# Optimization experiments

Measured on AMD Instinct MI355X. Metric: run time of the kernel, lower is better.

The kernel has to match this reference:

```python
import jax, jax.numpy as jnp
import numpy as np

B, S, D, H, HD = 2, 2048, 1024, 16, 64
K, L = 1024, 4  # num_codes, vq_levels


def setup_inputs() -> dict:
    key = jax.random.key(0)
    ks = jax.random.split(key, 12)
    w = lambda k, shape: jax.random.normal(k, shape, jnp.float32) * 0.02
    return {
        "x": jax.random.normal(ks[0], (B, S, D), jnp.float32),
        "ln1_g": jnp.ones((D,), jnp.float32), "ln1_b": jnp.zeros((D,), jnp.float32),
        "wq": w(ks[1], (D, D)), "wk": w(ks[2], (D, D)), "wv": w(ks[3], (D, D)),
        "wg": w(ks[4], (D, D)), "wo": w(ks[5], (D, D)),
        "ln2_g": jnp.ones((D,), jnp.float32), "ln2_b": jnp.zeros((D,), jnp.float32),
        "w1": w(ks[6], (D, 4 * D)), "b1": jnp.zeros((4 * D,), jnp.float32),
        "w2": w(ks[7], (4 * D, D)), "b2": jnp.zeros((D,), jnp.float32),
        "ln3_g": jnp.ones((D,), jnp.float32), "ln3_b": jnp.zeros((D,), jnp.float32),
        "codebooks": jax.random.uniform(ks[8], (L, K, D), jnp.float32, -1.0 / K, 1.0 / K),
    }


def _ln(x, g, b):
    m = jnp.mean(x, -1, keepdims=True)
    v = jnp.var(x, -1, keepdims=True)
    return (x - m) / jnp.sqrt(v + 1e-5) * g + b


def _rope(x):  # x: [B, S, H, HD]
    hd = x.shape[-1]
    inv = 1.0 / (10000.0 ** (jnp.arange(0, hd, 2, dtype=jnp.float32) / hd))
    t = jnp.arange(x.shape[1], dtype=jnp.float32)
    f = jnp.einsum('i,j->ij', t, inv)               # [S, HD/2]
    emb = jnp.concatenate([f, f], -1)               # [S, HD]
    cos = jnp.cos(emb)[None, :, None, :]
    sin = jnp.sin(emb)[None, :, None, :]
    x1, x2 = jnp.split(x, 2, -1)
    rot = jnp.concatenate([-x2, x1], -1)
    return x * cos + rot * sin


def reference(x, ln1_g, ln1_b, wq, wk, wv, wg, wo, ln2_g, ln2_b,
              w1, b1, w2, b2, ln3_g, ln3_b, codebooks):
    # --- retention sub-block (pre-LN) ---
    h = _ln(x, ln1_g, ln1_b)
    q = (h @ wq).reshape(B, S, H, HD)
    k = (h @ wk).reshape(B, S, H, HD)
    v = (h @ wv).reshape(B, S, H, HD)
    q, k = _rope(q), _rope(k)
    q, k, v = (a.transpose(0, 2, 1, 3) for a in (q, k, v))  # [B,H,S,HD]
    i = jnp.arange(S)
    dmask = jnp.tril(i[:, None] - i[None, :]).astype(jnp.float32)  # [S,S], >=0
    gamma = (1.0 - jnp.exp2(-5.0 - jnp.arange(H, dtype=jnp.float32)))[:, None, None]
    decay = (gamma ** dmask) * jnp.tril(jnp.ones((S, S), jnp.float32))  # [H,S,S]
    ret = jnp.einsum('bhqd,bhkd->bhqk', q, k) / np.sqrt(HD).astype(np.float32) * decay
    o = jnp.einsum('bhqk,bhkd->bhqd', ret, v).transpose(0, 2, 1, 3).reshape(B, S, D)
    g = jax.nn.silu(h @ wg)
    x = x + (o * g) @ wo
    # --- MLP sub-block (pre-LN) ---
    h2 = _ln(x, ln2_g, ln2_b)
    x = x + (jax.nn.gelu(h2 @ w1 + b1, approximate=False) @ w2 + b2)
    # --- residual vector quantizer ---
    xn = _ln(x, ln3_g, ln3_b)
    residual, total = xn, jnp.zeros_like(xn)
    ql, el = 0.0, 0.0
    for lvl in range(L):
        cb = codebooks[lvl]                         # [K, D]
        flat = residual.reshape(-1, D)              # [B*S, D]
        d2 = (jnp.sum(flat ** 2, 1, keepdims=True)
              + jnp.sum(cb ** 2, 1) - 2.0 * flat @ cb.T)
        idx = jnp.argmin(d2, 1)
        quant = cb[idx].reshape(xn.shape)
        ql = ql + jnp.mean((quant - jax.lax.stop_gradient(residual)) ** 2)
        el = el + jnp.mean((jax.lax.stop_gradient(quant) - residual) ** 2)
        total = total + quant
        residual = residual - jax.lax.stop_gradient(quant)
    final = xn + jax.lax.stop_gradient(total - xn)  # straight-through
    return (x + final, ql / L, el / L)
```

## Files before the change

### kernel.cpp

```cpp
#include <hip/hip_runtime.h>
#include <cstdint>
#include <cstddef>

#define DEV __device__ __forceinline__

typedef __attribute__((ext_vector_type(8))) short bf16x8;
typedef __attribute__((ext_vector_type(4))) float f32x4;

typedef const __attribute__((address_space(1))) void gl_void;
typedef __attribute__((address_space(3))) void lds_void;

DEV unsigned short f2bf(float f){
  union { float f; uint32_t u; } v; v.f = f;
  uint32_t r = v.u + 0x7FFFu + ((v.u >> 16) & 1u);
  return (unsigned short)(r >> 16);
}
DEV float bf2f(unsigned short u){
  union { uint32_t u; float f; } v; v.u = ((uint32_t)u) << 16; return v.f;
}
DEV uint32_t packbf2(float a, float b){
  return (uint32_t)f2bf(a) | ((uint32_t)f2bf(b) << 16);
}

__global__ void ln_kernel(const float* __restrict__ x, const float* __restrict__ gw,
                          const float* __restrict__ bw, unsigned short* __restrict__ obf,
                          float* __restrict__ of32)
{
  const int row = blockIdx.x, t = threadIdx.x;
  const float4 v = ((const float4*)(x + (size_t)row*1024))[t];
  float s  = v.x + v.y + v.z + v.w;
  float s2 = v.x*v.x + v.y*v.y + v.z*v.z + v.w*v.w;
  #pragma unroll
  for (int o = 32; o >= 1; o >>= 1){ s += __shfl_down(s, o); s2 += __shfl_down(s2, o); }
  __shared__ float red[8];
  const int w = t >> 6, ln = t & 63;
  if (ln == 0){ red[w] = s; red[4+w] = s2; }
  __syncthreads();
  const float fs  = red[0]+red[1]+red[2]+red[3];
  const float fs2 = red[4]+red[5]+red[6]+red[7];
  const float mean = fs * (1.0f/1024.0f);
  const float var  = fs2 * (1.0f/1024.0f) - mean*mean;
  const float rstd = rsqrtf(var + 1e-5f);
  const float4 gv = ((const float4*)gw)[t];
  const float4 bv = ((const float4*)bw)[t];
  float4 o4;
  o4.x = (v.x-mean)*rstd*gv.x + bv.x;
  o4.y = (v.y-mean)*rstd*gv.y + bv.y;
  o4.z = (v.z-mean)*rstd*gv.z + bv.z;
  o4.w = (v.w-mean)*rstd*gv.w + bv.w;
  if (of32) ((float4*)(of32 + (size_t)row*1024))[t] = o4;
  ushort4 ob; ob.x = f2bf(o4.x); ob.y = f2bf(o4.y); ob.z = f2bf(o4.z); ob.w = f2bf(o4.w);
  ((ushort4*)(obf + (size_t)row*1024))[t] = ob;
}

struct Ptr5 { const float* p[5]; };
__global__ void transpose_cvt5(Ptr5 in, unsigned short* __restrict__ out)
{
  __shared__ float tile[32][33];
  const float* src = in.p[blockIdx.z];
  unsigned short* dst = out + (size_t)blockIdx.z*1048576;
  const int c0 = blockIdx.x*32, r0 = blockIdx.y*32;
  const int tx = threadIdx.x & 31, ty = threadIdx.x >> 5;
  #pragma unroll
  for (int i = 0; i < 32; i += 8)
    tile[ty+i][tx] = src[(size_t)(r0+ty+i)*1024 + c0 + tx];
  __syncthreads();
  #pragma unroll
  for (int i = 0; i < 32; i += 8)
    dst[(size_t)(c0+ty+i)*1024 + r0 + tx] = f2bf(tile[tx][ty+i]);
}

__global__ void transpose_cvt(const float* __restrict__ in, unsigned short* __restrict__ out,
                              int R, int C)
{
  __shared__ float tile[32][33];
  const int c0 = blockIdx.x*32, r0 = blockIdx.y*32;
  const int tx = threadIdx.x & 31, ty = threadIdx.x >> 5;
  #pragma unroll
  for (int i = 0; i < 32; i += 8)
    tile[ty+i][tx] = in[(size_t)(r0+ty+i)*C + c0 + tx];
  __syncthreads();
  #pragma unroll
  for (int i = 0; i < 32; i += 8)
    out[(size_t)(c0+ty+i)*R + r0 + tx] = f2bf(tile[tx][ty+i]);
}

__global__ void cvtnorm_kernel(const float* __restrict__ cb, unsigned short* __restrict__ cbbf,
                               float* __restrict__ cbn2)
{
  const int code = blockIdx.x, t = threadIdx.x;
  const float4 v = ((const float4*)(cb + (size_t)code*1024))[t];
  ushort4 o; o.x = f2bf(v.x); o.y = f2bf(v.y); o.z = f2bf(v.z); o.w = f2bf(v.w);
  ((ushort4*)(cbbf + (size_t)code*1024))[t] = o;
  float s = v.x*v.x + v.y*v.y + v.z*v.z + v.w*v.w;
  #pragma unroll
  for (int off = 32; off >= 1; off >>= 1) s += __shfl_down(s, off);
  __shared__ float red[4];
  if ((t & 63) == 0) red[t >> 6] = s;
  __syncthreads();
  if (t == 0) cbn2[code] = red[0]+red[1]+red[2]+red[3];
}

__global__ void rope_tab(float2* __restrict__ rt)
{
  const int i = blockIdx.x*256 + threadIdx.x;
  const int s = i >> 5, j = i & 31;
  const float ang = (float)s * exp2f(-(float)j * 0.4152410118609203f);
  float sn, cs; sincosf(ang, &sn, &cs);
  rt[i] = make_float2(cs, sn);
}

template<int EPI>
__global__ __launch_bounds__(512, 2) void gemm256(
    const unsigned short* __restrict__ A, const unsigned short* __restrict__ BT,
    unsigned short* __restrict__ C, const float* __restrict__ bias,
    const float2* __restrict__ rt, int M, int N, int K)
{
  __shared__ __align__(16) unsigned short SH[65536];
  const int t = threadIdx.x;
  const int w = t >> 6, ln = t & 63, lg = ln >> 4, lc = ln & 15;
  const int wm = w >> 2, wn = w & 3;
  const int gx = gridDim.x, nwg = gridDim.x * gridDim.y;
  int lin = blockIdx.y * gx + blockIdx.x;
  lin = (lin >> 3) + (lin & 7) * (nwg >> 3);
  const int m0 = (lin / gx) * 256, n0 = (lin % gx) * 256;
  const int NT = K >> 6;
  const int nit = NT >> 1;

  f32x4 acc[2][2][4][2] = {};
  bf16x8 aF[4][2], bF[2][2];

  auto stageHT = [&](int d, int isB, int h, int kt){
    const unsigned short* src = isB ? BT : A;
    const int mb = (isB ? n0 : m0) + h*128;
    const int base16 = isB*4096 + d*2048 + h*1024;
    #pragma unroll
    for (int j = 0; j < 2; ++j){
      const int o = j*512 + t;
      const int wu = o & 63;
      const int r16 = wu >> 2, cu = wu & 3;
      const int s = o >> 6;
      const int rg = s >> 1, cg = s & 1;
      const int row = rg*16 + r16;
      const int srcu = cg*4 + (cu ^ ((r16 & 8) >> 2));
      __builtin_amdgcn_global_load_lds(
        (gl_void*)(src + (size_t)(mb + row)*K + (size_t)kt*64 + srcu*8),
        (lds_void*)&SH[(base16 + j*512 + (t & ~63))*8], 16, 0, 0);
    }
  };

  auto ldA = [&](int d, int mh, int mf, int ks) -> bf16x8 {
    const int u = d*2048 + mh*1024 + ((wm*4+mf)*2 + ks)*64 + lc*4 + (lg ^ ((lc & 8) >> 2));
    return *(const bf16x8*)&SH[u*8];
  };
  auto ldB = [&](int d, int nh, int nf, int ks) -> bf16x8 {
    const int u = 4096 + d*2048 + nh*1024 + ((wn*2+nf)*2 + ks)*64 + lc*4 + (lg ^ ((lc & 8) >> 2));
    return *(const bf16x8*)&SH[u*8];
  };

#define RD_A(d, mh) { _Pragma("unroll") for (int mf = 0; mf < 4; ++mf){ \
    aF[mf][0] = ldA(d, mh, mf, 0); aF[mf][1] = ldA(d, mh, mf, 1); } }
#define RD_B(d, nh) { _Pragma("unroll") for (int nf = 0; nf < 2; ++nf){ \
    bF[nf][0] = ldB(d, nh, nf, 0); bF[nf][1] = ldB(d, nh, nf, 1); } }
#define MM(mh, nh) { \
    __builtin_amdgcn_s_setprio(1); \
    _Pragma("unroll") for (int mf = 0; mf < 4; ++mf) \
      _Pragma("unroll") for (int nf = 0; nf < 2; ++nf){ \
        acc[mh][nh][mf][nf] = __builtin_amdgcn_mfma_f32_16x16x32_bf16(aF[mf][0], bF[nf][0], acc[mh][nh][mf][nf], 0, 0, 0); \
        acc[mh][nh][mf][nf] = __builtin_amdgcn_mfma_f32_16x16x32_bf16(aF[mf][1], bF[nf][1], acc[mh][nh][mf][nf], 0, 0, 0); } \
    __builtin_amdgcn_s_setprio(0); }
#define BAR()   __builtin_amdgcn_s_barrier()
#define LGKM0() asm volatile("s_waitcnt lgkmcnt(0)" ::: "memory")

  stageHT(0,0,0,0); stageHT(0,0,1,0); stageHT(0,1,0,0); stageHT(0,1,1,0);
  stageHT(1,0,0,1); stageHT(1,1,1,1);
  asm volatile("s_waitcnt vmcnt(4)" ::: "memory");
  BAR();

  for (int it = 0; it < nit; ++it){
    const int v = 2*it + 1, up = 2*it + 2, vp = 2*it + 3;
    const bool hu = (up < NT), hv = (vp < NT);

    RD_A(0,0); RD_B(0,0);
    stageHT(1,0,1,v);
    BAR(); LGKM0(); MM(0,0); BAR();

    RD_B(0,1);
    stageHT(1,1,0,v);
    BAR(); LGKM0(); MM(0,1); BAR();

    RD_A(0,1);
    if (hu) stageHT(0,0,0,up);
    BAR(); LGKM0(); MM(1,1); BAR();

    RD_B(0,0);
    if (hu) stageHT(0,1,1,up);
    BAR(); LGKM0(); MM(1,0);
    if (hu) asm volatile("s_waitcnt vmcnt(4)" ::: "memory");
    else    asm volatile("s_waitcnt vmcnt(0)" ::: "memory");
    BAR();

    RD_A(1,0); RD_B(1,0);
    if (hu) stageHT(0,0,1,up);
    BAR(); LGKM0(); MM(0,0); BAR();

    RD_B(1,1);
    if (hu) stageHT(0,1,0,up);
    BAR(); LGKM0(); MM(0,1); BAR();

    RD_A(1,1);
    if (hv) stageHT(1,0,0,vp);
    BAR(); LGKM0(); MM(1,1); BAR();

    RD_B(1,0);
    if (hv) stageHT(1,1,1,vp);
    BAR(); LGKM0(); MM(1,0);
    if (hv) asm volatile("s_waitcnt vmcnt(4)" ::: "memory");
    else    asm volatile("s_waitcnt vmcnt(0)" ::: "memory");
    BAR();
  }
#undef RD_A
#undef RD_B
#undef MM

  const int sect = n0 >> 10;
  unsigned short* outp3 = C + (size_t)sect*4194304;
  const int cb1 = n0 & 1023;
  unsigned short* slab = &SH[wm*4096];

  #pragma unroll
  for (int mh = 0; mh < 2; ++mh){
    #pragma unroll
    for (int mf = 0; mf < 4; ++mf){
      BAR();
      #pragma unroll
      for (int nh = 0; nh < 2; ++nh)
        #pragma unroll
        for (int nf = 0; nf < 2; ++nf)
          #pragma unroll
          for (int r = 0; r < 4; ++r){
            const int rho = lg*4 + r;
            const int c = nh*128 + wn*32 + nf*16 + lc;
            float vv = acc[mh][nh][mf][nf][r];
            if constexpr (EPI == 2){
              vv += bias[n0 + c];
              vv = 0.5f * vv * (1.0f + erff(vv * 0.70710678118654752f));
            }
            if constexpr (EPI == 3){ if (sect == 3) vv = vv * (1.0f / (1.0f + __expf(-vv))); }
            slab[rho*256 + ((((c>>3) ^ (rho&3)))<<3) + (c&7)] = f2bf(vv);
          }
      LGKM0();
      BAR();
      const int rr = ln >> 2;
      const int row = m0 + mh*128 + wm*64 + mf*16 + rr;
      #pragma unroll
      for (int kk = 0; kk < 2; ++kk){
        const int cc = wn*64 + (ln & 3)*16 + kk*8;
        const int u = cc >> 3;
        const bf16x8 vown = *(const bf16x8*)&slab[rr*256 + ((u ^ (rr&3))<<3)];
        if constexpr (EPI == 3){
          if (sect <= 1){
            const bf16x8 vpart = *(const bf16x8*)&slab[rr*256 + (((u^4) ^ (rr&3))<<3)];
            const int s_ = row & 2047;
            union { bf16x8 v; unsigned short s[8]; } ov, pv, res;
            ov.v = vown; pv.v = vpart;
            #pragma unroll
            for (int j = 0; j < 8; ++j){
              const int col = cc + j;
              const float2 cs = rt[(s_ << 5) + (col & 31)];
              const float a = bf2f(ov.s[j]), b = bf2f(pv.s[j]);
              res.s[j] = f2bf((col & 32) ? (a*cs.x + b*cs.y) : (a*cs.x - b*cs.y));
            }
            *(bf16x8*)(outp3 + (size_t)row*1024 + cb1 + cc) = res.v;
          } else {
            *(bf16x8*)(outp3 + (size_t)row*1024 + cb1 + cc) = vown;
          }
        } else {
          *(bf16x8*)(C + (size_t)row*N + n0 + cc) = vown;
        }
      }
    }
  }
#undef BAR
#undef LGKM0
}

template<int EPI, bool BIAS, bool RES, bool OUTBF, int NSPLIT>
__global__ __launch_bounds__(256, 3) void gemm64_bt(
    const unsigned short* __restrict__ A, const unsigned short* __restrict__ BT,
    void* __restrict__ Cv, const float* __restrict__ bias, const float* __restrict__ resid,
    int M, int N, int K)
{
  __shared__ __align__(16) unsigned short As[2][64*64];
  __shared__ __align__(16) unsigned short Bs[2][128*64];
  const int t = threadIdx.x;
  const int w = t >> 6, ln = t & 63, lg = ln >> 4, lc = ln & 15;
  const int gx = gridDim.x, nwg = gridDim.x * gridDim.y;
  int lin = blockIdx.y * gx + blockIdx.x;
  lin = (lin >> 3) + (lin & 7) * (nwg >> 3);
  const int bx = lin % gx, by = lin / gx;
  const int m0 = by * 64, n0 = bx * 128;
  const int wr = (w >> 1) * 32, wc = (w & 1) * 64;
  f32x4 acc[2][4] = {};
  const int nkt = (K >> 6) / NSPLIT;
  const int ktb = (NSPLIT > 1) ? blockIdx.z * nkt : 0;

  auto stage = [&](int buf, int kt){
    #pragma unroll
    for (int c = 0; c < 2; ++c){
      const int chunk = c*256 + t;
      const int row = chunk >> 3;
      const int kb = (((chunk & 7) << 4) ^ ((row & 7) << 4)) >> 1;
      __builtin_amdgcn_global_load_lds(
          (gl_void*)(A + (size_t)(m0+row)*K + (size_t)(ktb+kt)*64 + kb),
          (lds_void*)&As[buf][(c*256 + w*64)*8], 16, 0, 0);
    }
    #pragma unroll
    for (int c = 0; c < 4; ++c){
      const int chunk = c*256 + t;
      const int row = chunk >> 3;
      const int kb = (((chunk & 7) << 4) ^ ((row & 7) << 4)) >> 1;
      __builtin_amdgcn_global_load_lds(
          (gl_void*)(BT + (size_t)(n0+row)*K + (size_t)(ktb+kt)*64 + kb),
          (lds_void*)&Bs[buf][(c*256 + w*64)*8], 16, 0, 0);
    }
  };

  stage(0, 0);
  __syncthreads();
  for (int kt = 0; kt < nkt; ++kt){
    const int cur = kt & 1;
    if (kt + 1 < nkt) stage(cur ^ 1, kt + 1);
    #pragma unroll
    for (int ks = 0; ks < 2; ++ks){
      bf16x8 af[2], bfr[4];
      #pragma unroll
      for (int i = 0; i < 2; ++i){
        const int rowA = wr + i*16 + lc;
        const int colA = (((ks<<6) + (lg<<4)) ^ ((rowA & 7) << 4)) >> 1;
        af[i] = *(const bf16x8*)&As[cur][rowA*64 + colA];
      }
      #pragma unroll
      for (int i = 0; i < 4; ++i){
        const int rowB = wc + i*16 + lc;
        const int colB = (((ks<<6) + (lg<<4)) ^ ((rowB & 7) << 4)) >> 1;
        bfr[i] = *(const bf16x8*)&Bs[cur][rowB*64 + colB];
      }
      #pragma unroll
      for (int m = 0; m < 2; ++m)
        #pragma unroll
        for (int n = 0; n < 4; ++n)
          acc[m][n] = __builtin_amdgcn_mfma_f32_16x16x32_bf16(af[m], bfr[n], acc[m][n], 0, 0, 0);
    }
    __syncthreads();
  }

  if constexpr (EPI == 4){
    #pragma unroll
    for (int m = 0; m < 2; ++m){
      #pragma unroll
      for (int r = 0; r < 4; ++r){
        float best = 3.4e38f; int bi = 0;
        #pragma unroll
        for (int n = 0; n < 4; ++n){
          const int col = n0 + wc + n*16 + lc;
          const float d = bias[col] - 2.0f*acc[m][n][r];
          if (d < best){ best = d; bi = col; }
        }
        #pragma unroll
        for (int o = 1; o < 16; o <<= 1){
          const float ob = __shfl_xor(best, o);
          const int oi = __shfl_xor(bi, o);
          if (ob < best || (ob == best && oi < bi)){ best = ob; bi = oi; }
        }
        if (lc == 0){
          const int row = m0 + wr + m*16 + lg*4 + r;
          ((float2*)Cv)[row*16 + bx*2 + (w & 1)] = make_float2(best, (float)bi);
        }
      }
    }
    return;
  }

  float* Cp = (float*)Cv + (NSPLIT > 1 ? (size_t)blockIdx.z * (size_t)M * N : 0);
  #pragma unroll
  for (int m = 0; m < 2; ++m){
    #pragma unroll
    for (int n = 0; n < 4; ++n){
      #pragma unroll
      for (int r = 0; r < 4; ++r){
        const int row = m0 + wr + m*16 + lg*4 + r;
        const int col = n0 + wc + n*16 + lc;
        float v = acc[m][n][r];
        if constexpr (BIAS) v += bias[col];
        if constexpr (RES) v += resid[(size_t)row*N + col];
        if constexpr (OUTBF) ((unsigned short*)Cv)[(size_t)row*N + col] = f2bf(v);
        else                 Cp[(size_t)row*N + col] = v;
      }
    }
  }
}

__global__ void splitk_reduce(const float* __restrict__ p, const float* __restrict__ bias,
                              const float* __restrict__ resid, float* __restrict__ out)
{
  const int i = blockIdx.x*256 + threadIdx.x;
  const float4 a = ((const float4*)p)[i];
  const float4 b = ((const float4*)(p + 4194304))[i];
  const float4 rv = ((const float4*)resid)[i];
  const float4 bv = ((const float4*)bias)[i & 255];
  float4 o;
  o.x = a.x + b.x + rv.x + bv.x;
  o.y = a.y + b.y + rv.y + bv.y;
  o.z = a.z + b.z + rv.z + bv.z;
  o.w = a.w + b.w + rv.w + bv.w;
  ((float4*)out)[i] = o;
}

__global__ __launch_bounds__(256, 2) void chunk_sum(
    const unsigned short* __restrict__ kb, const unsigned short* __restrict__ vb,
    float* __restrict__ Tbuf)
{
  __shared__ unsigned short KT[64*72];
  __shared__ unsigned short VT[64*72];
  const int t = threadIdx.x, w = t >> 6, ln = t & 63, lg = ln >> 4, lc = ln & 15;
  const int blk = blockIdx.x;
  const int bh = blk >> 5, c = blk & 31;
  const int b = bh >> 4, hh = bh & 15;
  const float lg2g = log2f(1.0f - exp2f(-5.0f - (float)hh));
  #pragma unroll
  for (int ch = 0; ch < 2; ++ch){
    const int chunk = ch*256 + t;
    const int i = chunk >> 3, d0 = (chunk & 7)*8;
    const size_t gofs = ((size_t)(b*2048 + c*64 + i))*1024 + hh*64 + d0;
    const float wi = exp2f(lg2g * (float)(64 - i));
    union {uint4 u; unsigned short s[8];} kv, vv;
    kv.u = *(const uint4*)(kb + gofs);
    vv.u = *(const uint4*)(vb + gofs);
    #pragma unroll
    for (int j = 0; j < 8; ++j){
      KT[(d0+j)*72 + i] = f2bf(bf2f(kv.s[j]) * wi);
      VT[(d0+j)*72 + i] = vv.s[j];
    }
  }
  __syncthreads();
  f32x4 acc[4] = {};
  #pragma unroll
  for (int ks = 0; ks < 2; ++ks){
    const bf16x8 af = *(const bf16x8*)&KT[(w*16 + lc)*72 + ks*32 + lg*8];
    #pragma unroll
    for (int n = 0; n < 4; ++n){
      const bf16x8 bf = *(const bf16x8*)&VT[(n*16 + lc)*72 + ks*32 + lg*8];
      acc[n] = __builtin_amdgcn_mfma_f32_16x16x32_bf16(af, bf, acc[n], 0, 0, 0);
    }
  }
  float* out = Tbuf + (size_t)blk*4096;
  #pragma unroll
  for (int n = 0; n < 4; ++n)
    #pragma unroll
    for (int r = 0; r < 4; ++r)
      out[(w*16 + lg*4 + r)*64 + n*16 + lc] = acc[n][r];
}

__global__ void chunk_scan(const float* __restrict__ Tbuf, unsigned short* __restrict__ statesT)
{
  const int bh = blockIdx.x, q = blockIdx.y, t = threadIdx.x;
  const int hh = bh & 15;
  const float gamma = 1.0f - exp2f(-5.0f - (float)hh);
  const float g64 = exp2f(log2f(gamma) * 64.0f);
  float S[4] = {0.f, 0.f, 0.f, 0.f};
  const int dv = t >> 2;
  const int j0 = q*16 + (t & 3)*4;
  for (int c = 0; c < 32; ++c){
    const size_t base = ((size_t)(bh*32 + c))*4096;
    ushort4 p; p.x = f2bf(S[0]); p.y = f2bf(S[1]); p.z = f2bf(S[2]); p.w = f2bf(S[3]);
    *(ushort4*)(statesT + base + dv*64 + j0) = p;
    #pragma unroll
    for (int j = 0; j < 4; ++j)
      S[j] = g64*S[j] + Tbuf[base + (size_t)(j0 + j)*64 + dv];
  }
}

__global__ __launch_bounds__(256, 2) void retention_chunk(
    const unsigned short* __restrict__ qb, const unsigned short* __restrict__ kb,
    const unsigned short* __restrict__ vb, const unsigned short* __restrict__ gb,
    const unsigned short* __restrict__ statesT, unsigned short* __restrict__ og)
{
  __shared__ unsigned short VT[64*72];
  __shared__ unsigned short Pw[64*72];
  const int t = threadIdx.x, w = t >> 6, ln = t & 63, lg = ln >> 4, lc = ln & 15;
  const int blk = blockIdx.x;
  const int bh = blk >> 5, c = blk & 31;
  const int b = bh >> 4, hh = bh & 15;
  const float lg2g = log2f(1.0f - exp2f(-5.0f - (float)hh));
  float gpr[4];
  #pragma unroll
  for (int r = 0; r < 4; ++r) gpr[r] = exp2f(-lg2g * (float)r);
  const size_t rowbase = (size_t)(b*2048 + c*64);

  #pragma unroll
  for (int ch = 0; ch < 2; ++ch){
    const int chunk = ch*256 + t;
    const int i = chunk >> 3, d0 = (chunk & 7)*8;
    union {uint4 u; unsigned short s[8];} vv;
    vv.u = *(const uint4*)(vb + (rowbase + i)*1024 + hh*64 + d0);
    #pragma unroll
    for (int j = 0; j < 8; ++j) VT[(d0+j)*72 + i] = vv.s[j];
  }

  bf16x8 Qf[2], Kf[4][2];
  #pragma unroll
  for (int ks = 0; ks < 2; ++ks){
    union {uint4 u; bf16x8 f;} cv;
    cv.u = *(const uint4*)(qb + (rowbase + w*16 + lc)*1024 + hh*64 + ks*32 + lg*8);
    Qf[ks] = cv.f;
    #pragma unroll
    for (int mt = 0; mt < 4; ++mt){
      union {uint4 u; bf16x8 f;} kv;
      kv.u = *(const uint4*)(kb + (rowbase + mt*16 + lc)*1024 + hh*64 + ks*32 + lg*8);
      Kf[mt][ks] = kv.f;
    }
  }

  f32x4 st[4] = {};
  #pragma unroll
  for (int ks = 0; ks < 2; ++ks)
    #pragma unroll
    for (int mt = 0; mt < 4; ++mt)
      st[mt] = __builtin_amdgcn_mfma_f32_16x16x32_bf16(Kf[mt][ks], Qf[ks], st[mt], 0, 0, 0);

  __syncthreads();

  #pragma unroll
  for (int mt = 0; mt < 4; ++mt){
    const int kp = mt*16 + lg*4;
    const int qrow = w*16 + lc;
    const int delta0 = qrow - kp;
    const float dec0 = exp2f(lg2g * (float)delta0) * 0.125f;
    float vals[4];
    #pragma unroll
    for (int r = 0; r < 4; ++r)
      vals[r] = (delta0 >= r) ? st[mt][r] * dec0 * gpr[r] : 0.0f;
    uint2 pk; pk.x = packbf2(vals[0], vals[1]); pk.y = packbf2(vals[2], vals[3]);
    *(uint2*)&Pw[qrow*72 + kp] = pk;
  }

  f32x4 acc[4] = {};
  const unsigned short* Sbase = statesT + (size_t)blk*4096;
  #pragma unroll
  for (int ks = 0; ks < 2; ++ks)
    #pragma unroll
    for (int n = 0; n < 4; ++n){
      union {uint4 u; bf16x8 f;} sv;
      sv.u = *(const uint4*)(Sbase + (n*16 + lc)*64 + ks*32 + lg*8);
      acc[n] = __builtin_amdgcn_mfma_f32_16x16x32_bf16(Qf[ks], sv.f, acc[n], 0, 0, 0);
    }
  #pragma unroll
  for (int n = 0; n < 4; ++n)
    #pragma unroll
    for (int r = 0; r < 4; ++r)
      acc[n][r] *= exp2f(lg2g * (float)(w*16 + lg*4 + r)) * 0.125f;

  #pragma unroll
  for (int ks = 0; ks < 2; ++ks){
    const bf16x8 Pf = *(const bf16x8*)&Pw[(w*16 + lc)*72 + ks*32 + lg*8];
    #pragma unroll
    for (int n = 0; n < 4; ++n){
      const bf16x8 Vf = *(const bf16x8*)&VT[(n*16 + lc)*72 + ks*32 + lg*8];
      acc[n] = __builtin_amdgcn_mfma_f32_16x16x32_bf16(Pf, Vf, acc[n], 0, 0, 0);
    }
  }

  #pragma unroll
  for (int n = 0; n < 4; ++n){
    #pragma unroll
    for (int r = 0; r < 4; ++r){
      const size_t row = rowbase + w*16 + lg*4 + r;
      const int col = hh*64 + n*16 + lc;
      const float gv = bf2f(gb[row*1024 + col]);
      og[row*1024 + col] = f2bf(acc[n][r] * gv);
    }
  }
}

template<int FINAL>
__global__ void rvq_update3(const float* __restrict__ cb_l, const float2* __restrict__ partials,
                            const float* __restrict__ res_in, float* __restrict__ res_out,
                            unsigned short* __restrict__ resb, float* __restrict__ qlpart, int lvl,
                            const float* __restrict__ x2, const float* __restrict__ xn,
                            float* __restrict__ outf)
{
  const int m = blockIdx.x, t = threadIdx.x;
  __shared__ int sid;
  if (t == 0){
    float best = 3.4e38f; int bi = 0;
    #pragma unroll
    for (int p = 0; p < 16; ++p){
      const float2 pr = partials[m*16 + p];
      if (pr.x < best){ best = pr.x; bi = (int)pr.y; }
    }
    sid = bi;
  }
  __syncthreads();
  const int id = sid;
  const float4 qv = ((const float4*)(cb_l + (size_t)id*1024))[t];
  const float4 rv = ((const float4*)(res_in + (size_t)m*1024))[t];
  float4 nr; nr.x = rv.x - qv.x; nr.y = rv.y - qv.y; nr.z = rv.z - qv.z; nr.w = rv.w - qv.w;
  if constexpr (FINAL){
    const float4 a = ((const float4*)(x2 + (size_t)m*1024))[t];
    const float4 b = ((const float4*)(xn + (size_t)m*1024))[t];
    float4 o;
    o.x = a.x + b.x - nr.x;
    o.y = a.y + b.y - nr.y;
    o.z = a.z + b.z - nr.z;
    o.w = a.w + b.w - nr.w;
    ((float4*)(outf + (size_t)m*1024))[t] = o;
  } else {
    ((float4*)(res_out + (size_t)m*1024))[t] = nr;
    ushort4 nb; nb.x = f2bf(nr.x); nb.y = f2bf(nr.y); nb.z = f2bf(nr.z); nb.w = f2bf(nr.w);
    ((ushort4*)(resb + (size_t)m*1024))[t] = nb;
  }
  float s = nr.x*nr.x + nr.y*nr.y + nr.z*nr.z + nr.w*nr.w;
  #pragma unroll
  for (int o = 32; o >= 1; o >>= 1) s += __shfl_down(s, o);
  __shared__ float red[4];
  if ((t & 63) == 0) red[t >> 6] = s;
  __syncthreads();
  if (t == 0) qlpart[lvl*4096 + m] = red[0]+red[1]+red[2]+red[3];
}

__global__ void ql_final(const float* __restrict__ qlpart, float* __restrict__ outs)
{
  const int t = threadIdx.x;
  float s = 0.f;
  for (int i = t; i < 16384; i += 256) s += qlpart[i];
  #pragma unroll
  for (int o = 32; o >= 1; o >>= 1) s += __shfl_down(s, o);
  __shared__ float red[4];
  if ((t & 63) == 0) red[t >> 6] = s;
  __syncthreads();
  if (t == 0){
    const float q = (red[0]+red[1]+red[2]+red[3]) * (1.0f/4194304.0f) * 0.25f;
    outs[0] = q; outs[1] = q;
  }
}

extern "C" void kernel_launch(void* const* d_in, const int* in_sizes, int n_in,
                              void* d_out, int out_size, void* d_ws, size_t ws_size,
                              hipStream_t stream)
{
  const float* x     = (const float*)d_in[0];
  const float* ln1_g = (const float*)d_in[1];
  const float* ln1_b = (const float*)d_in[2];
  const float* wq    = (const float*)d_in[3];
  const float* wk    = (const float*)d_in[4];
  const float* wv    = (const float*)d_in[5];
  const float* wg    = (const float*)d_in[6];
  const float* wo    = (const float*)d_in[7];
  const float* ln2_g = (const float*)d_in[8];
  const float* ln2_b = (const float*)d_in[9];
  const float* w1    = (const float*)d_in[10];
  const float* b1    = (const float*)d_in[11];
  const float* w2    = (const float*)d_in[12];
  const float* b2    = (const float*)d_in[13];
  const float* ln3_g = (const float*)d_in[14];
  const float* ln3_b = (const float*)d_in[15];
  const float* cb    = (const float*)d_in[16];

  char* ws = (char*)d_ws;
  const size_t MB = 1024*1024;
  unsigned short* wqkvgT = (unsigned short*)(ws + 0*MB);
  unsigned short* w1T  = (unsigned short*)(ws + 10*MB);
  unsigned short* w2T  = (unsigned short*)(ws + 18*MB);
  unsigned short* cbbf = (unsigned short*)(ws + 26*MB);
  float* cbn2     = (float*)(ws + 34*MB);
  float* qlpart   = (float*)(ws + 34*MB + 16*1024);
  float2* partials= (float2*)(ws + 34*MB + 128*1024);
  unsigned short* hbf  = (unsigned short*)(ws + 35*MB);
  unsigned short* qbuf = (unsigned short*)(ws + 43*MB);
  unsigned short* kbuf = (unsigned short*)(ws + 51*MB);
  unsigned short* vbuf = (unsigned short*)(ws + 59*MB);
  unsigned short* gbuf = (unsigned short*)(ws + 67*MB);
  float* skbuf  = (float*)(ws + 43*MB);
  unsigned short* ogb  = (unsigned short*)(ws + 75*MB);
  float* x1     = (float*)(ws + 83*MB);
  unsigned short* h2   = (unsigned short*)(ws + 99*MB);
  unsigned short* a1   = (unsigned short*)(ws + 107*MB);
  float* x2     = (float*)(ws + 139*MB);
  float* Tbuf   = (float*)(ws + 139*MB);
  float* xnf    = (float*)(ws + 155*MB);
  unsigned short* statesT = (unsigned short*)(ws + 155*MB);
  unsigned short* resb = (unsigned short*)(ws + 171*MB);
  float2* rtab  = (float2*)(ws + 179*MB);
  float* resw   = (float*)(ws + 187*MB);

  float* outf = (float*)d_out;

  Ptr5 p5; p5.p[0]=wq; p5.p[1]=wk; p5.p[2]=wv; p5.p[3]=wg; p5.p[4]=wo;
  hipLaunchKernelGGL(transpose_cvt5, dim3(32,32,5), dim3(256), 0, stream, p5, wqkvgT);
  hipLaunchKernelGGL(transpose_cvt, dim3(128,32), dim3(256), 0, stream, w1, w1T, 1024, 4096);
  hipLaunchKernelGGL(transpose_cvt, dim3(32,128), dim3(256), 0, stream, w2, w2T, 4096, 1024);
  hipLaunchKernelGGL(cvtnorm_kernel, dim3(4096), dim3(256), 0, stream, cb, cbbf, cbn2);
  hipLaunchKernelGGL(rope_tab, dim3(256), dim3(256), 0, stream, rtab);

  hipLaunchKernelGGL(ln_kernel, dim3(4096), dim3(256), 0, stream, x, ln1_g, ln1_b, hbf, (float*)nullptr);
  hipLaunchKernelGGL((gemm256<3>), dim3(16,16), dim3(512), 0, stream,
                     hbf, wqkvgT, qbuf, (const float*)nullptr, (const float2*)rtab, 4096, 4096, 1024);
  hipLaunchKernelGGL(chunk_sum,  dim3(1024), dim3(256), 0, stream, kbuf, vbuf, Tbuf);
  hipLaunchKernelGGL(chunk_scan, dim3(32,4), dim3(256), 0, stream, Tbuf, statesT);
  hipLaunchKernelGGL(retention_chunk, dim3(1024), dim3(256), 0, stream,
                     qbuf, kbuf, vbuf, gbuf, statesT, ogb);
  hipLaunchKernelGGL((gemm64_bt<0,false,true,false,1>), dim3(8,64), dim3(256), 0, stream,
                     ogb, wqkvgT + 4194304, (void*)x1, (const float*)nullptr, x, 4096, 1024, 1024);

  hipLaunchKernelGGL(ln_kernel, dim3(4096), dim3(256), 0, stream, x1, ln2_g, ln2_b, h2, (float*)nullptr);
  hipLaunchKernelGGL((gemm256<2>), dim3(16,16), dim3(512), 0, stream,
                     h2, w1T, a1, b1, (const float2*)rtab, 4096, 4096, 1024);
  hipLaunchKernelGGL((gemm64_bt<0,false,false,false,2>), dim3(8,64,2), dim3(256), 0, stream,
                     a1, w2T, (void*)skbuf, (const float*)nullptr, (const float*)nullptr, 4096, 1024, 4096);
  hipLaunchKernelGGL(splitk_reduce, dim3(4096), dim3(256), 0, stream, skbuf, b2, x1, x2);

  hipLaunchKernelGGL(ln_kernel, dim3(4096), dim3(256), 0, stream, x2, ln3_g, ln3_b, resb, xnf);
  for (int lvl = 0; lvl < 4; ++lvl){
    hipLaunchKernelGGL((gemm64_bt<4,false,false,false,1>), dim3(8,64), dim3(256), 0, stream,
                       resb, cbbf + (size_t)lvl*1048576, (void*)partials,
                       cbn2 + lvl*1024, (const float*)nullptr, 4096, 1024, 1024);
    if (lvl < 3)
      hipLaunchKernelGGL((rvq_update3<0>), dim3(4096), dim3(256), 0, stream,
                         cb + (size_t)lvl*1048576, partials,
                         (lvl == 0) ? xnf : resw, resw, resb, qlpart, lvl,
                         (const float*)nullptr, (const float*)nullptr, (float*)nullptr);
    else
      hipLaunchKernelGGL((rvq_update3<1>), dim3(4096), dim3(256), 0, stream,
                         cb + (size_t)lvl*1048576, partials,
                         resw, (float*)nullptr, (unsigned short*)nullptr, qlpart, lvl,
                         x2, xnf, outf);
  }

  hipLaunchKernelGGL(ql_final, dim3(1), dim3(256), 0, stream, qlpart, outf + 4194304);
}
```

Measured before the change: 404.7 us.

## Add 128x128 split-K GEMM for MLP down-projection and merge prep kernels

```diff
diff --git a/kernel.cpp b/kernel.cpp
--- a/kernel.cpp
+++ b/kernel.cpp
@@ -54,60 +54,56 @@
 }
 
 struct Ptr5 { const float* p[5]; };
-__global__ void transpose_cvt5(Ptr5 in, unsigned short* __restrict__ out)
+
+DEV void dev_transpose(const float* __restrict__ src, unsigned short* __restrict__ dst,
+                       int r0, int c0, int R, int C)
 {
   __shared__ float tile[32][33];
-  const float* src = in.p[blockIdx.z];
-  unsigned short* dst = out + (size_t)blockIdx.z*1048576;
-  const int c0 = blockIdx.x*32, r0 = blockIdx.y*32;
   const int tx = threadIdx.x & 31, ty = threadIdx.x >> 5;
   #pragma unroll
   for (int i = 0; i < 32; i += 8)
-    tile[ty+i][tx] = src[(size_t)(r0+ty+i)*1024 + c0 + tx];
+    tile[ty+i][tx] = src[(size_t)(r0+ty+i)*C + c0 + tx];
   __syncthreads();
   #pragma unroll
   for (int i = 0; i < 32; i += 8)
-    dst[(size_t)(c0+ty+i)*1024 + r0 + tx] = f2bf(tile[tx][ty+i]);
-}
-
-__global__ void transpose_cvt(const float* __restrict__ in, unsigned short* __restrict__ out,
-                              int R, int C)
-{
-  __shared__ float tile[32][33];
-  const int c0 = blockIdx.x*32, r0 = blockIdx.y*32;
-  const int tx = threadIdx.x & 31, ty = threadIdx.x >> 5;
-  #pragma unroll
-  for (int i = 0; i < 32; i += 8)
-    tile[ty+i][tx] = in[(size_t)(r0+ty+i)*C + c0 + tx];
-  __syncthreads();
-  #pragma unroll
-  for (int i = 0; i < 32; i += 8)
-    out[(size_t)(c0+ty+i)*R + r0 + tx] = f2bf(tile[tx][ty+i]);
-}
-
-__global__ void cvtnorm_kernel(const float* __restrict__ cb, unsigned short* __restrict__ cbbf,
-                               float* __restrict__ cbn2)
-{
-  const int code = blockIdx.x, t = threadIdx.x;
-  const float4 v = ((const float4*)(cb + (size_t)code*1024))[t];
-  ushort4 o; o.x = f2bf(v.x); o.y = f2bf(v.y); o.z = f2bf(v.z); o.w = f2bf(v.w);
-  ((ushort4*)(cbbf + (size_t)code*1024))[t] = o;
-  float s = v.x*v.x + v.y*v.y + v.z*v.z + v.w*v.w;
-  #pragma unroll
-  for (int off = 32; off >= 1; off >>= 1) s += __shfl_down(s, off);
-  __shared__ float red[4];
-  if ((t & 63) == 0) red[t >> 6] = s;
-  __syncthreads();
-  if (t == 0) cbn2[code] = red[0]+red[1]+red[2]+red[3];
-}
-
-__global__ void rope_tab(float2* __restrict__ rt)
-{
-  const int i = blockIdx.x*256 + threadIdx.x;
-  const int s = i >> 5, j = i & 31;
-  const float ang = (float)s * exp2f(-(float)j * 0.4152410118609203f);
-  float sn, cs; sincosf(ang, &sn, &cs);
-  rt[i] = make_float2(cs, sn);
+    dst[(size_t)(c0+ty+i)*R + r0 + tx] = f2bf(tile[tx][ty+i]);
+}
+
+__global__ void prep_all(Ptr5 p5, unsigned short* __restrict__ wqkvgT,
+                         const float* __restrict__ w1, unsigned short* __restrict__ w1T,
+                         const float* __restrict__ w2, unsigned short* __restrict__ w2T,
+                         const float* __restrict__ cb, unsigned short* __restrict__ cbbf,
+                         float* __restrict__ cbn2, float2* __restrict__ rtab)
+{
+  const int b = blockIdx.x, t = threadIdx.x;
+  if (b < 5120){
+    const int z = b >> 10, r = b & 1023;
+    dev_transpose(p5.p[z], wqkvgT + (size_t)z*1048576, (r >> 5)*32, (r & 31)*32, 1024, 1024);
+  } else if (b < 9216){
+    const int r = b - 5120;
+    dev_transpose(w1, w1T, (r >> 7)*32, (r & 127)*32, 1024, 4096);
+  } else if (b < 13312){
+    const int r = b - 9216;
+    dev_transpose(w2, w2T, (r >> 5)*32, (r & 31)*32, 4096, 1024);
+  } else if (b < 17408){
+    const int code = b - 13312;
+    const float4 v = ((const float4*)(cb + (size_t)code*1024))[t];
+    ushort4 o; o.x = f2bf(v.x); o.y = f2bf(v.y); o.z = f2bf(v.z); o.w = f2bf(v.w);
+    ((ushort4*)(cbbf + (size_t)code*1024))[t] = o;
+    float s = v.x*v.x + v.y*v.y + v.z*v.z + v.w*v.w;
+    #pragma unroll
+    for (int off = 32; off >= 1; off >>= 1) s += __shfl_down(s, off);
+    __shared__ float red[4];
+    if ((t & 63) == 0) red[t >> 6] = s;
+    __syncthreads();
+    if (t == 0) cbn2[code] = red[0]+red[1]+red[2]+red[3];
+  } else {
+    const int i = (b - 17408)*256 + t;
+    const int s = i >> 5, j = i & 31;
+    const float ang = (float)s * exp2f(-(float)j * 0.4152410118609203f);
+    float sn, cs; sincosf(ang, &sn, &cs);
+    rtab[i] = make_float2(cs, sn);
+  }
 }
 
 template<int EPI>
@@ -285,7 +281,71 @@
 #undef LGKM0
 }
 
-template<int EPI, bool BIAS, bool RES, bool OUTBF, int NSPLIT>
+template<int NSPLIT>
+__global__ __launch_bounds__(256, 4) void gemm128_sk(
+    const unsigned short* __restrict__ A, const unsigned short* __restrict__ BT,
+    float* __restrict__ Cp_base, int M, int N, int K)
+{
+  __shared__ __align__(16) unsigned short As[2][128*32];
+  __shared__ __align__(16) unsigned short Bs[2][128*32];
+  const int t = threadIdx.x;
+  const int w = t >> 6, ln = t & 63, lg = ln >> 4, lc = ln & 15;
+  const int gx = gridDim.x, nwg = gridDim.x * gridDim.y;
+  int lin = blockIdx.y * gx + blockIdx.x;
+  lin = (lin >> 3) + (lin & 7) * (nwg >> 3);
+  const int m0 = (lin / gx) * 128, n0 = (lin % gx) * 128;
+  const int wr = (w >> 1) * 64, wc = (w & 1) * 64;
+  f32x4 acc[4][4] = {};
+  const int nkt = (K >> 5) / NSPLIT;
+  const int ktb = blockIdx.z * nkt;
+
+  auto stage = [&](int buf, int kt){
+    #pragma unroll
+    for (int c = 0; c < 2; ++c){
+      const int chunk = c*256 + t;
+      const int row = chunk >> 2, ke = (chunk & 3) * 8;
+      __builtin_amdgcn_global_load_lds(
+          (gl_void*)(A + (size_t)(m0+row)*K + (size_t)(ktb+kt)*32 + ke),
+          (lds_void*)&As[buf][(c*256 + w*64)*8], 16, 0, 0);
+      __builtin_amdgcn_global_load_lds(
+          (gl_void*)(BT + (size_t)(n0+row)*K + (size_t)(ktb+kt)*32 + ke),
+          (lds_void*)&Bs[buf][(c*256 + w*64)*8], 16, 0, 0);
+    }
+  };
+
+  stage(0, 0);
+  __syncthreads();
+  for (int kt = 0; kt < nkt; ++kt){
+    const int cur = kt & 1;
+    if (kt + 1 < nkt) stage(cur ^ 1, kt + 1);
+    bf16x8 af[4], bfr[4];
+    #pragma unroll
+    for (int i = 0; i < 4; ++i){
+      af[i]  = *(const bf16x8*)&As[cur][(wr + i*16 + lc)*32 + lg*8];
+      bfr[i] = *(const bf16x8*)&Bs[cur][(wc + i*16 + lc)*32 + lg*8];
+    }
+    #pragma unroll
+    for (int m = 0; m < 4; ++m)
+      #pragma unroll
+      for (int n = 0; n < 4; ++n)
+        acc[m][n] = __builtin_amdgcn_mfma_f32_16x16x32_bf16(af[m], bfr[n], acc[m][n], 0, 0, 0);
+    __syncthreads();
+  }
+
+  float* Cp = Cp_base + (size_t)blockIdx.z * (size_t)M * N;
+  #pragma unroll
+  for (int m = 0; m < 4; ++m)
+    #pragma unroll
+    for (int n = 0; n < 4; ++n)
+      #pragma unroll
+      for (int r = 0; r < 4; ++r){
+        const int row = m0 + wr + m*16 + lg*4 + r;
+        const int col = n0 + wc + n*16 + lc;
+        Cp[(size_t)row*N + col] = acc[m][n][r];
+      }
+}
+
+template<int EPI, bool BIAS, bool RES, bool OUTBF>
 __global__ __launch_bounds__(256, 3) void gemm64_bt(
     const unsigned short* __restrict__ A, const unsigned short* __restrict__ BT,
     void* __restrict__ Cv, const float* __restrict__ bias, const float* __restrict__ resid,
@@ -302,8 +362,7 @@
   const int m0 = by * 64, n0 = bx * 128;
   const int wr = (w >> 1) * 32, wc = (w & 1) * 64;
   f32x4 acc[2][4] = {};
-  const int nkt = (K >> 6) / NSPLIT;
-  const int ktb = (NSPLIT > 1) ? blockIdx.z * nkt : 0;
+  const int nkt = K >> 6;
 
   auto stage = [&](int buf, int kt){
     #pragma unroll
@@ -312,7 +371,7 @@
       const int row = chunk >> 3;
       const int kb = (((chunk & 7) << 4) ^ ((row & 7) << 4)) >> 1;
       __builtin_amdgcn_global_load_lds(
-          (gl_void*)(A + (size_t)(m0+row)*K + (size_t)(ktb+kt)*64 + kb),
+          (gl_void*)(A + (size_t)(m0+row)*K + (size_t)kt*64 + kb),
           (lds_void*)&As[buf][(c*256 + w*64)*8], 16, 0, 0);
     }
     #pragma unroll
@@ -321,7 +380,7 @@
       const int row = chunk >> 3;
       const int kb = (((chunk & 7) << 4) ^ ((row & 7) << 4)) >> 1;
       __builtin_amdgcn_global_load_lds(
-          (gl_void*)(BT + (size_t)(n0+row)*K + (size_t)(ktb+kt)*64 + kb),
+          (gl_void*)(BT + (size_t)(n0+row)*K + (size_t)kt*64 + kb),
           (lds_void*)&Bs[buf][(c*256 + w*64)*8], 16, 0, 0);
     }
   };
@@ -382,7 +441,6 @@
     return;
   }
 
-  float* Cp = (float*)Cv + (NSPLIT > 1 ? (size_t)blockIdx.z * (size_t)M * N : 0);
   #pragma unroll
   for (int m = 0; m < 2; ++m){
     #pragma unroll
@@ -395,7 +453,7 @@
         if constexpr (BIAS) v += bias[col];
         if constexpr (RES) v += resid[(size_t)row*N + col];
         if constexpr (OUTBF) ((unsigned short*)Cv)[(size_t)row*N + col] = f2bf(v);
-        else                 Cp[(size_t)row*N + col] = v;
+        else                 ((float*)Cv)[(size_t)row*N + col] = v;
       }
     }
   }
@@ -697,11 +755,8 @@
   float* outf = (float*)d_out;
 
   Ptr5 p5; p5.p[0]=wq; p5.p[1]=wk; p5.p[2]=wv; p5.p[3]=wg; p5.p[4]=wo;
-  hipLaunchKernelGGL(transpose_cvt5, dim3(32,32,5), dim3(256), 0, stream, p5, wqkvgT);
-  hipLaunchKernelGGL(transpose_cvt, dim3(128,32), dim3(256), 0, stream, w1, w1T, 1024, 4096);
-  hipLaunchKernelGGL(transpose_cvt, dim3(32,128), dim3(256), 0, stream, w2, w2T, 4096, 1024);
-  hipLaunchKernelGGL(cvtnorm_kernel, dim3(4096), dim3(256), 0, stream, cb, cbbf, cbn2);
-  hipLaunchKernelGGL(rope_tab, dim3(256), dim3(256), 0, stream, rtab);
+  hipLaunchKernelGGL(prep_all, dim3(17664), dim3(256), 0, stream,
+                     p5, wqkvgT, w1, w1T, w2, w2T, cb, cbbf, cbn2, rtab);
 
   hipLaunchKernelGGL(ln_kernel, dim3(4096), dim3(256), 0, stream, x, ln1_g, ln1_b, hbf, (float*)nullptr);
   hipLaunchKernelGGL((gemm256<3>), dim3(16,16), dim3(512), 0, stream,
@@ -710,19 +765,19 @@
   hipLaunchKernelGGL(chunk_scan, dim3(32,4), dim3(256), 0, stream, Tbuf, statesT);
   hipLaunchKernelGGL(retention_chunk, dim3(1024), dim3(256), 0, stream,
                      qbuf, kbuf, vbuf, gbuf, statesT, ogb);
-  hipLaunchKernelGGL((gemm64_bt<0,false,true,false,1>), dim3(8,64), dim3(256), 0, stream,
+  hipLaunchKernelGGL((gemm64_bt<0,false,true,false>), dim3(8,64), dim3(256), 0, stream,
                      ogb, wqkvgT + 4194304, (void*)x1, (const float*)nullptr, x, 4096, 1024, 1024);
 
   hipLaunchKernelGGL(ln_kernel, dim3(4096), dim3(256), 0, stream, x1, ln2_g, ln2_b, h2, (float*)nullptr);
   hipLaunchKernelGGL((gemm256<2>), dim3(16,16), dim3(512), 0, stream,
                      h2, w1T, a1, b1, (const float2*)rtab, 4096, 4096, 1024);
-  hipLaunchKernelGGL((gemm64_bt<0,false,false,false,2>), dim3(8,64,2), dim3(256), 0, stream,
-                     a1, w2T, (void*)skbuf, (const float*)nullptr, (const float*)nullptr, 4096, 1024, 4096);
+  hipLaunchKernelGGL((gemm128_sk<2>), dim3(8,32,2), dim3(256), 0, stream,
+                     a1, w2T, skbuf, 4096, 1024, 4096);
   hipLaunchKernelGGL(splitk_reduce, dim3(4096), dim3(256), 0, stream, skbuf, b2, x1, x2);
 
   hipLaunchKernelGGL(ln_kernel, dim3(4096), dim3(256), 0, stream, x2, ln3_g, ln3_b, resb, xnf);
   for (int lvl = 0; lvl < 4; ++lvl){
-    hipLaunchKernelGGL((gemm64_bt<4,false,false,false,1>), dim3(8,64), dim3(256), 0, stream,
+    hipLaunchKernelGGL((gemm64_bt<4,false,false,false>), dim3(8,64), dim3(256), 0, stream,
                        resb, cbbf + (size_t)lvl*1048576, (void*)partials,
                        cbn2 + lvl*1024, (const float*)nullptr, 4096, 1024, 1024);
     if (lvl < 3)
```

Result: faster. 392.8 us (-2.9%).
